# Performance work log

Hardware: AMD Instinct MI355X
Metric: run time of the kernel (lower is better)

The kernel has to match this reference:

```python
import jax, jax.numpy as jnp
import numpy as np

D_MODEL = 1024
NUM_HEADS = 16
D_K = D_MODEL // NUM_HEADS  # 64
THETA = 10000.0
BATCH = 2
SEQ = 2048


def _rope_tables(positions, d_k, theta):
    # freq_k = theta**(-2k/d_k), each repeated twice (interleaved layout)
    k = jnp.arange(d_k // 2, dtype=jnp.float32)
    freq = theta ** (-2.0 * k / d_k)            # [d_k/2]
    freq = jnp.repeat(freq, 2)                  # [d_k], pattern f0,f0,f1,f1,...
    ang = positions.astype(jnp.float32)[:, None] * freq[None, :]  # [s, d_k]
    return jnp.cos(ang), jnp.sin(ang)


def _apply_rope(x, cos, sin):
    # x: [b, h, s, d_k]; interleaved rotation: y[0::2]=-x[1::2], y[1::2]=x[0::2]
    x1 = x[..., 0::2]
    x2 = x[..., 1::2]
    y = jnp.stack([-x2, x1], axis=-1).reshape(x.shape)
    return x * cos + y * sin


def setup_inputs() -> dict:
    key = jax.random.key(0)
    kx, kq, kk, kv, ko = jax.random.split(key, 5)
    sw = (2.0 / (2 * D_MODEL)) ** 0.5
    return {
        "x": jax.random.normal(kx, (BATCH, SEQ, D_MODEL), dtype=jnp.float32),
        "WQ": jax.random.normal(kq, (D_MODEL, D_MODEL), dtype=jnp.float32) * sw,
        "WK": jax.random.normal(kk, (D_MODEL, D_MODEL), dtype=jnp.float32) * sw,
        "WV": jax.random.normal(kv, (D_MODEL, D_MODEL), dtype=jnp.float32) * sw,
        "WO": jax.random.normal(ko, (D_MODEL, D_MODEL), dtype=jnp.float32) * sw,
        "token_positions": jnp.arange(SEQ, dtype=jnp.int32),
    }


def reference(x, WQ, WK, WV, WO, token_positions):
    b, s, d_model = x.shape
    h, d_k = NUM_HEADS, D_K

    # fused QKV projection: W = cat([WQ,WK,WV], 0); QKV = x @ W.T
    W = jnp.concatenate([WQ, WK, WV], axis=0)          # [3*d_model, d_model]
    QKV = jnp.einsum('bsd,ed->bse', x, W)              # [b, s, 3*d_model]
    Q, K, V = jnp.split(QKV, 3, axis=-1)               # each [b, s, d_model]

    def to_heads(t):
        return t.reshape(b, s, h, d_k).transpose(0, 2, 1, 3)  # [b, h, s, d_k]

    Q, K, V = to_heads(Q), to_heads(K), to_heads(V)

    cos, sin = _rope_tables(token_positions, d_k, THETA)       # [s, d_k]
    Q = _apply_rope(Q, cos, sin)
    K = _apply_rope(K, cos, sin)

    scale = 1.0 / jnp.sqrt(jnp.float32(d_k))
    scores = jnp.einsum('bhqd,bhkd->bhqk', Q, K) * scale       # [b,h,s,s]
    causal = jnp.tril(jnp.ones((s, s), dtype=bool))
    scores = jnp.where(causal[None, None], scores, -jnp.inf)
    probs = jax.nn.softmax(scores, axis=-1)
    attn = jnp.einsum('bhqk,bhkd->bhqd', probs, V)             # [b,h,s,d_k]
    attn = attn.transpose(0, 2, 1, 3).reshape(b, s, h * d_k)   # [b,s,d_model]
    return jnp.einsum('bsd,ed->bse', attn, WO)                 # [b,s,d_model]
```

## Files before the change

kernel.cpp:

```cpp
#include <hip/hip_runtime.h>
#include <hip/hip_bf16.h>
#include <math.h>

#define BATCH 2
#define SEQ 2048
#define DMODEL 1024
#define NHEADS 16
#define DK 64
#define BH (BATCH*NHEADS)
#define GK 1024

#define SCALE2 0.18033688011112042f
#define SHIFT  16.0f

typedef __bf16 bf16_t;
typedef __bf16 bf16x8 __attribute__((ext_vector_type(8)));
typedef __bf16 bf16x4 __attribute__((ext_vector_type(4)));
typedef float  floatx4 __attribute__((ext_vector_type(4)));

__device__ __forceinline__ void load_lds16(const bf16_t* g, bf16_t* l) {
    __builtin_amdgcn_global_load_lds(
        (const __attribute__((address_space(1))) void*)g,
        (__attribute__((address_space(3))) void*)l,
        16, 0, 0);
}

__global__ __launch_bounds__(256) void rope_tables_kernel(
    const int* __restrict__ pos, float2* __restrict__ csT)
{
    int idx = blockIdx.x * 256 + threadIdx.x;
    int kk = idx & 31, s = idx >> 5;
    float freq = exp2f((float)kk * (-13.287712379549449f / 32.0f));
    float ang = (float)pos[s] * freq;
    float sn, cs;
    sincosf(ang, &sn, &cs);
    csT[idx] = make_float2(cs, sn);
}

__global__ __launch_bounds__(256) void convert_all_kernel(
    const float* __restrict__ x,
    const float* __restrict__ WQ, const float* __restrict__ WK,
    const float* __restrict__ WV, const float* __restrict__ WO,
    bf16_t* __restrict__ xb, bf16_t* __restrict__ Wb)
{
    const int blk = blockIdx.x;
    const float* src;
    bf16_t* dst;
    int base;
    if (blk < 2048) {
        src = x; dst = xb; base = blk * 2048;
    } else {
        int wi  = (blk - 2048) >> 9;
        base = ((blk - 2048) & 511) * 2048;
        src = (wi == 0) ? WQ : (wi == 1) ? WK : (wi == 2) ? WV : WO;
        dst = Wb + (size_t)wi * DMODEL * DMODEL;
    }
    int i = base + threadIdx.x * 8;
    float4 a = *(const float4*)(src + i);
    float4 b = *(const float4*)(src + i + 4);
    bf16x8 o;
    o[0] = (bf16_t)a.x; o[1] = (bf16_t)a.y; o[2] = (bf16_t)a.z; o[3] = (bf16_t)a.w;
    o[4] = (bf16_t)b.x; o[5] = (bf16_t)b.y; o[6] = (bf16_t)b.z; o[7] = (bf16_t)b.w;
    *(bf16x8*)(dst + i) = o;
}

__device__ __forceinline__ void gemm128_mainloop(
    const bf16_t* __restrict__ Arows, const bf16_t* __restrict__ Brows,
    bf16_t (*As)[32], bf16_t (*Bs)[32], int tid, floatx4 acc[4][4])
{
    const int lane = tid & 63;
    const int w = tid >> 6;
    const int wm = w >> 1, wn = w & 1;
    const int r = lane & 15, q = lane >> 4;

    const int row0 = tid >> 2,         kc0 = (tid & 3) << 3;
    const int row1 = (tid + 256) >> 2, kc1 = kc0;

    for (int kt = 0; kt < GK; kt += 32) {
        __syncthreads();
        load_lds16(Arows + (size_t)row0 * GK + kt + kc0, &As[row0][kc0]);
        load_lds16(Arows + (size_t)row1 * GK + kt + kc1, &As[row1][kc1]);
        load_lds16(Brows + (size_t)row0 * GK + kt + kc0, &Bs[row0][kc0]);
        load_lds16(Brows + (size_t)row1 * GK + kt + kc1, &Bs[row1][kc1]);
        __syncthreads();

        bf16x8 af[4], bfr[4];
        #pragma unroll
        for (int i = 0; i < 4; ++i)
            af[i] = *(const bf16x8*)&As[wm * 64 + i * 16 + r][q << 3];
        #pragma unroll
        for (int j = 0; j < 4; ++j)
            bfr[j] = *(const bf16x8*)&Bs[wn * 64 + j * 16 + r][q << 3];

        #pragma unroll
        for (int i = 0; i < 4; ++i)
            #pragma unroll
            for (int j = 0; j < 4; ++j)
                acc[i][j] = __builtin_amdgcn_mfma_f32_16x16x32_bf16(
                    af[i], bfr[j], acc[i][j], 0, 0, 0);
    }
}

__global__ __launch_bounds__(256) void qkv_gemm_kernel(
    const bf16_t* __restrict__ x, const bf16_t* __restrict__ Wb,
    const float2* __restrict__ csT,
    bf16_t* __restrict__ Qh, bf16_t* __restrict__ Kh, bf16_t* __restrict__ Vt)
{
    __shared__ __align__(16) char qsmem[128 * 136 * 2];
    bf16_t (*As)[32]  = (bf16_t(*)[32])qsmem;
    bf16_t (*Bs)[32]  = (bf16_t(*)[32])(qsmem + 8192);
    bf16_t (*Tt)[136] = (bf16_t(*)[136])qsmem;

    const int tid = threadIdx.x;
    const int m0 = blockIdx.y * 128;
    const int n0g = blockIdx.x * 128;
    const int which = n0g >> 10;
    const int nl0 = n0g & 1023;
    const bf16_t* Wsel = Wb + (size_t)which * DMODEL * DMODEL;

    floatx4 acc[4][4];
    #pragma unroll
    for (int i = 0; i < 4; ++i)
        #pragma unroll
        for (int j = 0; j < 4; ++j)
            acc[i][j] = (floatx4){0.f, 0.f, 0.f, 0.f};

    gemm128_mainloop(x + (size_t)m0 * GK, Wsel + (size_t)nl0 * GK, As, Bs, tid, acc);
    __syncthreads();

    const int w = tid >> 6, lane = tid & 63;
    const int wm = w >> 1, wn = w & 1;
    const int r = lane & 15, qd = lane >> 4;

    if (which < 2) {
        #pragma unroll
        for (int i = 0; i < 4; ++i)
            #pragma unroll
            for (int j = 0; j < 4; ++j)
                #pragma unroll
                for (int reg = 0; reg < 4; ++reg)
                    Tt[wm * 64 + i * 16 + qd * 4 + reg][wn * 64 + j * 16 + r] =
                        (bf16_t)acc[i][j][reg];
        __syncthreads();

        bf16_t* dst = (which == 0) ? Qh : Kh;
        #pragma unroll
        for (int k2 = 0; k2 < 8; ++k2) {
            int id = tid + 256 * k2;
            int rowm = id >> 4;
            int ch = id & 15;
            int m = m0 + rowm, b = m >> 11, s = m & 2047;
            int n = nl0 + ch * 8, h = n >> 6, dk = n & 63;
            bf16x8 v = *(const bf16x8*)&Tt[rowm][ch * 8];
            const float4* csp = (const float4*)&csT[(s << 5) + (dk >> 1)];
            float4 c01 = csp[0], c23 = csp[1];
            bf16x8 o;
            float e, od;
            e = (float)v[0]; od = (float)v[1];
            o[0] = (bf16_t)(e * c01.x - od * c01.y); o[1] = (bf16_t)(od * c01.x + e * c01.y);
            e = (float)v[2]; od = (float)v[3];
            o[2] = (bf16_t)(e * c01.z - od * c01.w); o[3] = (bf16_t)(od * c01.z + e * c01.w);
            e = (float)v[4]; od = (float)v[5];
            o[4] = (bf16_t)(e * c23.x - od * c23.y); o[5] = (bf16_t)(od * c23.x + e * c23.y);
            e = (float)v[6]; od = (float)v[7];
            o[6] = (bf16_t)(e * c23.z - od * c23.w); o[7] = (bf16_t)(od * c23.z + e * c23.w);
            *(bf16x8*)(dst + (((size_t)(b << 4) + h) * SEQ + s) * DK + dk) = o;
        }
    } else {
        #pragma unroll
        for (int i = 0; i < 4; ++i)
            #pragma unroll
            for (int j = 0; j < 4; ++j) {
                int n_local = wn * 64 + j * 16 + r;
                int m_base  = wm * 64 + i * 16 + qd * 4;
                bf16x4 t;
                #pragma unroll
                for (int reg = 0; reg < 4; ++reg) t[reg] = (bf16_t)acc[i][j][reg];
                *(bf16x4*)&Tt[n_local][m_base] = t;
            }
        __syncthreads();
        const int b = m0 >> 11, s0 = m0 & 2047;
        #pragma unroll
        for (int k2 = 0; k2 < 8; ++k2) {
            int id = tid + 256 * k2;
            int row = id >> 4;
            int ch  = id & 15;
            int n = nl0 + row, h = n >> 6, dk = n & 63;
            bf16x8 val = *(const bf16x8*)&Tt[row][ch * 8];
            *(bf16x8*)(Vt + (((size_t)(b << 4) + h) * DK + dk) * SEQ + s0 + ch * 8) = val;
        }
    }
}

__global__ __launch_bounds__(512, 4) void attn_mfma_kernel(
    const bf16_t* __restrict__ Qh, const bf16_t* __restrict__ Kh,
    const bf16_t* __restrict__ Vtg, bf16_t* __restrict__ attnO)
{
    __shared__ __align__(16) char smem[55296];
    bf16_t (*Ks)[64][72] = (bf16_t(*)[64][72])smem;
    bf16_t (*Vs)[64][72] = (bf16_t(*)[64][72])(smem + 18432);
    bf16_t (*ps)[16][72] = (bf16_t(*)[16][72])(smem + 36864);
    float  (*Om)[64][68] = (float(*)[64][68])smem;
    float  (*lsum)[64]   = (float(*)[64])(smem + 36864);

    const int tid = threadIdx.x, w = tid >> 6, lane = tid & 63;
    const int grp = w >> 2, wv = w & 3;
    const int r = lane & 15, qd = lane >> 4;
    const int bh = blockIdx.y;
    const int t = tid & 255;
    const int row0 = t >> 3, c80 = (t & 7) * 8;

    const bf16_t* Kbh = Kh  + (size_t)bh * SEQ * DK;
    const bf16_t* Vbh = Vtg + (size_t)bh * DK * SEQ;
    const int b = bh >> 4, h = bh & 15;

    for (int half = 0; half < 2; ++half) {
        const int qt = half ? (int)blockIdx.x : (31 - (int)blockIdx.x);
        const int q0 = qt * 64;
        const int nIter = (qt >> 1) + 1;

        const bf16_t* Qbase = Qh + (((size_t)bh * SEQ) + q0 + wv * 16 + r) * DK;
        bf16x8 aq0 = *(const bf16x8*)(Qbase + qd * 8);
        bf16x8 aq1 = *(const bf16x8*)(Qbase + 32 + qd * 8);

        int j0 = grp * 64;
        bf16x8 pk0 = *(const bf16x8*)(Kbh + (size_t)(j0 + row0) * DK + c80);
        bf16x8 pk1 = *(const bf16x8*)(Kbh + (size_t)(j0 + row0 + 32) * DK + c80);
        bf16x8 pv0 = *(const bf16x8*)(Vbh + (size_t)row0 * SEQ + j0 + c80);
        bf16x8 pv1 = *(const bf16x8*)(Vbh + (size_t)(row0 + 32) * SEQ + j0 + c80);

        floatx4 Oa[4];
        #pragma unroll
        for (int nd = 0; nd < 4; ++nd) Oa[nd] = (floatx4){0.f, 0.f, 0.f, 0.f};
        float l_lane[4] = {0.f, 0.f, 0.f, 0.f};

        for (int it = 0; it < nIter; ++it) {
            const int kb = 2 * it + grp;
            const bool active = (kb <= qt);
            __syncthreads();
            if (active) {
                *(bf16x8*)&Ks[grp][row0][c80]      = pk0;
                *(bf16x8*)&Ks[grp][row0 + 32][c80] = pk1;
                *(bf16x8*)&Vs[grp][row0][c80]      = pv0;
                *(bf16x8*)&Vs[grp][row0 + 32][c80] = pv1;
            }
            if (kb + 2 <= qt) {
                const int j0n = (kb + 2) * 64;
                pk0 = *(const bf16x8*)(Kbh + (size_t)(j0n + row0) * DK + c80);
                pk1 = *(const bf16x8*)(Kbh + (size_t)(j0n + row0 + 32) * DK + c80);
                pv0 = *(const bf16x8*)(Vbh + (size_t)row0 * SEQ + j0n + c80);
                pv1 = *(const bf16x8*)(Vbh + (size_t)(row0 + 32) * SEQ + j0n + c80);
            }
            __syncthreads();
            if (!active) continue;

            floatx4 acc[4];
            #pragma unroll
            for (int nt = 0; nt < 4; ++nt) {
                bf16x8 bk0 = *(const bf16x8*)&Ks[grp][nt * 16 + r][qd * 8];
                bf16x8 bk1 = *(const bf16x8*)&Ks[grp][nt * 16 + r][32 + qd * 8];
                floatx4 a = (floatx4){0.f, 0.f, 0.f, 0.f};
                a = __builtin_amdgcn_mfma_f32_16x16x32_bf16(aq0, bk0, a, 0, 0, 0);
                a = __builtin_amdgcn_mfma_f32_16x16x32_bf16(aq1, bk1, a, 0, 0, 0);
                acc[nt] = a;
            }

            const bool lastb = (kb == qt);
            #pragma unroll
            for (int nt = 0; nt < 4; ++nt)
                #pragma unroll
                for (int rg = 0; rg < 4; ++rg) {
                    float s2 = fmaf(acc[nt][rg], SCALE2, -SHIFT);
                    if (lastb && (nt * 16 + r > wv * 16 + qd * 4 + rg)) s2 = -200.0f;
                    float p = exp2f(s2);
                    acc[nt][rg] = p;
                    l_lane[rg] += p;
                }

            #pragma unroll
            for (int nt = 0; nt < 4; ++nt)
                #pragma unroll
                for (int rg = 0; rg < 4; ++rg)
                    ps[w][qd * 4 + rg][nt * 16 + r] = (bf16_t)acc[nt][rg];
            bf16x8 ap0 = *(const bf16x8*)&ps[w][r][qd * 8];
            bf16x8 ap1 = *(const bf16x8*)&ps[w][r][32 + qd * 8];

            #pragma unroll
            for (int nd = 0; nd < 4; ++nd) {
                bf16x8 bv0 = *(const bf16x8*)&Vs[grp][nd * 16 + r][qd * 8];
                bf16x8 bv1 = *(const bf16x8*)&Vs[grp][nd * 16 + r][32 + qd * 8];
                floatx4 c = Oa[nd];
                c = __builtin_amdgcn_mfma_f32_16x16x32_bf16(ap0, bv0, c, 0, 0, 0);
                c = __builtin_amdgcn_mfma_f32_16x16x32_bf16(ap1, bv1, c, 0, 0, 0);
                Oa[nd] = c;
            }
        }

        __syncthreads();
        #pragma unroll
        for (int rg = 0; rg < 4; ++rg) {
            float l = l_lane[rg];
            #pragma unroll
            for (int off = 1; off < 16; off <<= 1) l += __shfl_xor(l, off);
            int rowq = wv * 16 + qd * 4 + rg;
            if (r == 0) lsum[grp][rowq] = l;
            #pragma unroll
            for (int nd = 0; nd < 4; ++nd)
                Om[grp][rowq][nd * 16 + r] = Oa[nd][rg];
        }
        __syncthreads();
        {
            int rowq = tid >> 3, c8 = (tid & 7) * 8;
            float inv = 1.0f / (lsum[0][rowq] + lsum[1][rowq]);
            float4 a0 = *(const float4*)&Om[0][rowq][c8];
            float4 a1 = *(const float4*)&Om[0][rowq][c8 + 4];
            float4 b0 = *(const float4*)&Om[1][rowq][c8];
            float4 b1 = *(const float4*)&Om[1][rowq][c8 + 4];
            bf16x8 o;
            o[0] = (bf16_t)((a0.x + b0.x) * inv);
            o[1] = (bf16_t)((a0.y + b0.y) * inv);
            o[2] = (bf16_t)((a0.z + b0.z) * inv);
            o[3] = (bf16_t)((a0.w + b0.w) * inv);
            o[4] = (bf16_t)((a1.x + b1.x) * inv);
            o[5] = (bf16_t)((a1.y + b1.y) * inv);
            o[6] = (bf16_t)((a1.z + b1.z) * inv);
            o[7] = (bf16_t)((a1.w + b1.w) * inv);
            int s = q0 + rowq;
            *(bf16x8*)(attnO + ((size_t)b * SEQ + s) * DMODEL + (h << 6) + c8) = o;
        }
    }
}

__global__ __launch_bounds__(256) void out_gemm_kernel(
    const bf16_t* __restrict__ attnI, const bf16_t* __restrict__ WOb,
    float* __restrict__ out)
{
    __shared__ __align__(16) bf16_t As[64][32];
    __shared__ __align__(16) bf16_t Bs[128][32];

    const int tid = threadIdx.x;
    const int m0 = blockIdx.y * 64;
    const int n0 = blockIdx.x * 128;
    const int lane = tid & 63, w = tid >> 6;
    const int wm = w >> 1, wn = w & 1;
    const int r = lane & 15, q = lane >> 4;

    const bf16_t* Arows = attnI + (size_t)m0 * GK;
    const bf16_t* Brows = WOb + (size_t)n0 * GK;
    const int rowA = tid >> 2, kc = (tid & 3) << 3;
    const int rowB1 = (tid + 256) >> 2;

    floatx4 acc[2][4];
    #pragma unroll
    for (int i = 0; i < 2; ++i)
        #pragma unroll
        for (int j = 0; j < 4; ++j)
            acc[i][j] = (floatx4){0.f, 0.f, 0.f, 0.f};

    for (int kt = 0; kt < GK; kt += 32) {
        __syncthreads();
        load_lds16(Arows + (size_t)rowA * GK + kt + kc, &As[rowA][kc]);
        load_lds16(Brows + (size_t)rowA * GK + kt + kc, &Bs[rowA][kc]);
        load_lds16(Brows + (size_t)rowB1 * GK + kt + kc, &Bs[rowB1][kc]);
        __syncthreads();

        bf16x8 af[2], bfr[4];
        #pragma unroll
        for (int i = 0; i < 2; ++i)
            af[i] = *(const bf16x8*)&As[wm * 32 + i * 16 + r][q << 3];
        #pragma unroll
        for (int j = 0; j < 4; ++j)
            bfr[j] = *(const bf16x8*)&Bs[wn * 64 + j * 16 + r][q << 3];

        #pragma unroll
        for (int i = 0; i < 2; ++i)
            #pragma unroll
            for (int j = 0; j < 4; ++j)
                acc[i][j] = __builtin_amdgcn_mfma_f32_16x16x32_bf16(
                    af[i], bfr[j], acc[i][j], 0, 0, 0);
    }

    #pragma unroll
    for (int i = 0; i < 2; ++i)
        #pragma unroll
        for (int j = 0; j < 4; ++j)
            #pragma unroll
            for (int reg = 0; reg < 4; ++reg) {
                int m = m0 + wm * 32 + i * 16 + q * 4 + reg;
                int n = n0 + wn * 64 + j * 16 + r;
                out[(size_t)m * DMODEL + n] = acc[i][j][reg];
            }
}

extern "C" void kernel_launch(void* const* d_in, const int* in_sizes, int n_in,
                              void* d_out, int out_size, void* d_ws, size_t ws_size,
                              hipStream_t stream)
{
    (void)in_sizes; (void)n_in; (void)out_size; (void)ws_size;

    const float* x  = (const float*)d_in[0];
    const float* WQ = (const float*)d_in[1];
    const float* WK = (const float*)d_in[2];
    const float* WV = (const float*)d_in[3];
    const float* WO = (const float*)d_in[4];
    const int* tpos = (const int*)d_in[5];
    float* out = (float*)d_out;

    bf16_t* xb   = (bf16_t*)d_ws;
    bf16_t* Wb   = xb + (size_t)BATCH * SEQ * DMODEL;
    bf16_t* Qh   = Wb + (size_t)4 * DMODEL * DMODEL;
    bf16_t* Kh   = Qh + (size_t)BH * SEQ * DK;
    bf16_t* Vt   = Kh + (size_t)BH * SEQ * DK;
    bf16_t* attn = Vt + (size_t)BH * SEQ * DK;
    float2* csT  = (float2*)(attn + (size_t)BATCH * SEQ * DMODEL);

    rope_tables_kernel<<<dim3(SEQ * 32 / 256), dim3(256), 0, stream>>>(tpos, csT);

    convert_all_kernel<<<dim3(4096), dim3(256), 0, stream>>>(
        x, WQ, WK, WV, WO, xb, Wb);

    qkv_gemm_kernel<<<dim3(3 * DMODEL / 128, BATCH * SEQ / 128), dim3(256), 0, stream>>>(
        xb, Wb, csT, Qh, Kh, Vt);

    attn_mfma_kernel<<<dim3(16, 32), dim3(512), 0, stream>>>(Qh, Kh, Vt, attn);

    out_gemm_kernel<<<dim3(DMODEL / 128, BATCH * SEQ / 64), dim3(256), 0, stream>>>(
        attn, Wb + (size_t)3 * DMODEL * DMODEL, out);
}
```

Before: 184.3 us.

## Fuse rope-table build into conversion, co-process paired query tiles, split-K output GEMM

The rope cos/sin table is now built by extra blocks of the conversion kernel, which removes one launch. The attention kernel processes its high and low causal query tiles together in a single K/V loop, so each K/V tile loaded into LDS is reused by both tiles, at the cost of more registers and LDS. The output projection becomes a split-K GEMM with 128x128 tiles that writes two fp32 partials into a reused workspace, followed by a reduction kernel. This doubles the output traffic and adds a launch in exchange for larger tiles.

```diff
diff --git a/kernel.cpp b/kernel.cpp
--- a/kernel.cpp
+++ b/kernel.cpp
@@ -9,6 +9,8 @@
 #define DK 64
 #define BH (BATCH*NHEADS)
 #define GK 1024
+#define NX (BATCH*SEQ*DMODEL)
+#define NW (DMODEL*DMODEL)
 
 #define SCALE2 0.18033688011112042f
 #define SHIFT  16.0f
@@ -25,25 +27,24 @@
         16, 0, 0);
 }
 
-__global__ __launch_bounds__(256) void rope_tables_kernel(
-    const int* __restrict__ pos, float2* __restrict__ csT)
-{
-    int idx = blockIdx.x * 256 + threadIdx.x;
-    int kk = idx & 31, s = idx >> 5;
-    float freq = exp2f((float)kk * (-13.287712379549449f / 32.0f));
-    float ang = (float)pos[s] * freq;
-    float sn, cs;
-    sincosf(ang, &sn, &cs);
-    csT[idx] = make_float2(cs, sn);
-}
-
 __global__ __launch_bounds__(256) void convert_all_kernel(
     const float* __restrict__ x,
     const float* __restrict__ WQ, const float* __restrict__ WK,
     const float* __restrict__ WV, const float* __restrict__ WO,
-    bf16_t* __restrict__ xb, bf16_t* __restrict__ Wb)
+    const int* __restrict__ pos,
+    bf16_t* __restrict__ xb, bf16_t* __restrict__ Wb, float2* __restrict__ csT)
 {
     const int blk = blockIdx.x;
+    if (blk >= 4096) {
+        int idx = (blk - 4096) * 256 + threadIdx.x;
+        int kk = idx & 31, s = idx >> 5;
+        float freq = exp2f((float)kk * (-13.287712379549449f / 32.0f));
+        float ang = (float)pos[s] * freq;
+        float sn, cs;
+        sincosf(ang, &sn, &cs);
+        csT[idx] = make_float2(cs, sn);
+        return;
+    }
     const float* src;
     bf16_t* dst;
     int base;
@@ -53,7 +54,7 @@
         int wi  = (blk - 2048) >> 9;
         base = ((blk - 2048) & 511) * 2048;
         src = (wi == 0) ? WQ : (wi == 1) ? WK : (wi == 2) ? WV : WO;
-        dst = Wb + (size_t)wi * DMODEL * DMODEL;
+        dst = Wb + (size_t)wi * NW;
     }
     int i = base + threadIdx.x * 8;
     float4 a = *(const float4*)(src + i);
@@ -66,7 +67,7 @@
 
 __device__ __forceinline__ void gemm128_mainloop(
     const bf16_t* __restrict__ Arows, const bf16_t* __restrict__ Brows,
-    bf16_t (*As)[32], bf16_t (*Bs)[32], int tid, floatx4 acc[4][4])
+    bf16_t (*As)[32], bf16_t (*Bs)[32], int tid, floatx4 acc[4][4], int klen)
 {
     const int lane = tid & 63;
     const int w = tid >> 6;
@@ -76,7 +77,7 @@
     const int row0 = tid >> 2,         kc0 = (tid & 3) << 3;
     const int row1 = (tid + 256) >> 2, kc1 = kc0;
 
-    for (int kt = 0; kt < GK; kt += 32) {
+    for (int kt = 0; kt < klen; kt += 32) {
         __syncthreads();
         load_lds16(Arows + (size_t)row0 * GK + kt + kc0, &As[row0][kc0]);
         load_lds16(Arows + (size_t)row1 * GK + kt + kc1, &As[row1][kc1]);
@@ -116,7 +117,7 @@
     const int n0g = blockIdx.x * 128;
     const int which = n0g >> 10;
     const int nl0 = n0g & 1023;
-    const bf16_t* Wsel = Wb + (size_t)which * DMODEL * DMODEL;
+    const bf16_t* Wsel = Wb + (size_t)which * NW;
 
     floatx4 acc[4][4];
     #pragma unroll
@@ -125,7 +126,7 @@
         for (int j = 0; j < 4; ++j)
             acc[i][j] = (floatx4){0.f, 0.f, 0.f, 0.f};
 
-    gemm128_mainloop(x + (size_t)m0 * GK, Wsel + (size_t)nl0 * GK, As, Bs, tid, acc);
+    gemm128_mainloop(x + (size_t)m0 * GK, Wsel + (size_t)nl0 * GK, As, Bs, tid, acc, GK);
     __syncthreads();
 
     const int w = tid >> 6, lane = tid & 63;
@@ -147,8 +148,7 @@
         #pragma unroll
         for (int k2 = 0; k2 < 8; ++k2) {
             int id = tid + 256 * k2;
-            int rowm = id >> 4;
-            int ch = id & 15;
+            int rowm = id >> 4, ch = id & 15;
             int m = m0 + rowm, b = m >> 11, s = m & 2047;
             int n = nl0 + ch * 8, h = n >> 6, dk = n & 63;
             bf16x8 v = *(const bf16x8*)&Tt[rowm][ch * 8];
@@ -183,8 +183,7 @@
         #pragma unroll
         for (int k2 = 0; k2 < 8; ++k2) {
             int id = tid + 256 * k2;
-            int row = id >> 4;
-            int ch  = id & 15;
+            int row = id >> 4, ch = id & 15;
             int n = nl0 + row, h = n >> 6, dk = n & 63;
             bf16x8 val = *(const bf16x8*)&Tt[row][ch * 8];
             *(bf16x8*)(Vt + (((size_t)(b << 4) + h) * DK + dk) * SEQ + s0 + ch * 8) = val;
@@ -196,17 +195,19 @@
     const bf16_t* __restrict__ Qh, const bf16_t* __restrict__ Kh,
     const bf16_t* __restrict__ Vtg, bf16_t* __restrict__ attnO)
 {
-    __shared__ __align__(16) char smem[55296];
-    bf16_t (*Ks)[64][72] = (bf16_t(*)[64][72])smem;
-    bf16_t (*Vs)[64][72] = (bf16_t(*)[64][72])(smem + 18432);
-    bf16_t (*ps)[16][72] = (bf16_t(*)[16][72])(smem + 36864);
-    float  (*Om)[64][68] = (float(*)[64][68])smem;
-    float  (*lsum)[64]   = (float(*)[64])(smem + 36864);
+    __shared__ __align__(16) char smem[73728];
+    bf16_t (*Ks)[64][72]    = (bf16_t(*)[64][72])smem;
+    bf16_t (*Vs)[64][72]    = (bf16_t(*)[64][72])(smem + 18432);
+    bf16_t (*ps)[2][16][72] = (bf16_t(*)[2][16][72])(smem + 36864);
+    float  (*Om)[64][68]    = (float(*)[64][68])smem;
+    float  (*lsum)[64]      = (float(*)[64])(smem + 36864);
 
     const int tid = threadIdx.x, w = tid >> 6, lane = tid & 63;
     const int grp = w >> 2, wv = w & 3;
     const int r = lane & 15, qd = lane >> 4;
-    const int bh = blockIdx.y;
+    const int bh = blockIdx.y, bx = blockIdx.x;
+    const int qt_hi = 31 - bx, qt_lo = bx;
+    const int q0h = qt_hi * 64, q0l = qt_lo * 64;
     const int t = tid & 255;
     const int row0 = t >> 3, c80 = (t & 7) * 8;
 
@@ -214,99 +215,128 @@
     const bf16_t* Vbh = Vtg + (size_t)bh * DK * SEQ;
     const int b = bh >> 4, h = bh & 15;
 
-    for (int half = 0; half < 2; ++half) {
-        const int qt = half ? (int)blockIdx.x : (31 - (int)blockIdx.x);
-        const int q0 = qt * 64;
-        const int nIter = (qt >> 1) + 1;
-
-        const bf16_t* Qbase = Qh + (((size_t)bh * SEQ) + q0 + wv * 16 + r) * DK;
-        bf16x8 aq0 = *(const bf16x8*)(Qbase + qd * 8);
-        bf16x8 aq1 = *(const bf16x8*)(Qbase + 32 + qd * 8);
-
-        int j0 = grp * 64;
-        bf16x8 pk0 = *(const bf16x8*)(Kbh + (size_t)(j0 + row0) * DK + c80);
-        bf16x8 pk1 = *(const bf16x8*)(Kbh + (size_t)(j0 + row0 + 32) * DK + c80);
-        bf16x8 pv0 = *(const bf16x8*)(Vbh + (size_t)row0 * SEQ + j0 + c80);
-        bf16x8 pv1 = *(const bf16x8*)(Vbh + (size_t)(row0 + 32) * SEQ + j0 + c80);
-
-        floatx4 Oa[4];
-        #pragma unroll
-        for (int nd = 0; nd < 4; ++nd) Oa[nd] = (floatx4){0.f, 0.f, 0.f, 0.f};
-        float l_lane[4] = {0.f, 0.f, 0.f, 0.f};
-
-        for (int it = 0; it < nIter; ++it) {
-            const int kb = 2 * it + grp;
-            const bool active = (kb <= qt);
-            __syncthreads();
-            if (active) {
-                *(bf16x8*)&Ks[grp][row0][c80]      = pk0;
-                *(bf16x8*)&Ks[grp][row0 + 32][c80] = pk1;
-                *(bf16x8*)&Vs[grp][row0][c80]      = pv0;
-                *(bf16x8*)&Vs[grp][row0 + 32][c80] = pv1;
+    const bf16_t* Qbh = Qh + ((size_t)bh * SEQ + wv * 16 + r) * DK;
+    bf16x8 aqh0 = *(const bf16x8*)(Qbh + (size_t)q0h * DK + qd * 8);
+    bf16x8 aqh1 = *(const bf16x8*)(Qbh + (size_t)q0h * DK + 32 + qd * 8);
+    bf16x8 aql0 = *(const bf16x8*)(Qbh + (size_t)q0l * DK + qd * 8);
+    bf16x8 aql1 = *(const bf16x8*)(Qbh + (size_t)q0l * DK + 32 + qd * 8);
+
+    int j0 = grp * 64;
+    bf16x8 pk0 = *(const bf16x8*)(Kbh + (size_t)(j0 + row0) * DK + c80);
+    bf16x8 pk1 = *(const bf16x8*)(Kbh + (size_t)(j0 + row0 + 32) * DK + c80);
+    bf16x8 pv0 = *(const bf16x8*)(Vbh + (size_t)row0 * SEQ + j0 + c80);
+    bf16x8 pv1 = *(const bf16x8*)(Vbh + (size_t)(row0 + 32) * SEQ + j0 + c80);
+
+    floatx4 Oh[4], Ol[4];
+    #pragma unroll
+    for (int nd = 0; nd < 4; ++nd) {
+        Oh[nd] = (floatx4){0.f, 0.f, 0.f, 0.f};
+        Ol[nd] = (floatx4){0.f, 0.f, 0.f, 0.f};
+    }
+    float lh[4] = {0.f, 0.f, 0.f, 0.f}, ll[4] = {0.f, 0.f, 0.f, 0.f};
+
+    const int nIter = (qt_hi >> 1) + 1;
+    for (int it = 0; it < nIter; ++it) {
+        const int kb = 2 * it + grp;
+        const bool act = (kb <= qt_hi);
+        const bool lo_act = (kb <= qt_lo);
+        __syncthreads();
+        if (act) {
+            *(bf16x8*)&Ks[grp][row0][c80]      = pk0;
+            *(bf16x8*)&Ks[grp][row0 + 32][c80] = pk1;
+            *(bf16x8*)&Vs[grp][row0][c80]      = pv0;
+            *(bf16x8*)&Vs[grp][row0 + 32][c80] = pv1;
+        }
+        if (kb + 2 <= qt_hi) {
+            const int j0n = (kb + 2) * 64;
+            pk0 = *(const bf16x8*)(Kbh + (size_t)(j0n + row0) * DK + c80);
+            pk1 = *(const bf16x8*)(Kbh + (size_t)(j0n + row0 + 32) * DK + c80);
+            pv0 = *(const bf16x8*)(Vbh + (size_t)row0 * SEQ + j0n + c80);
+            pv1 = *(const bf16x8*)(Vbh + (size_t)(row0 + 32) * SEQ + j0n + c80);
+        }
+        __syncthreads();
+        if (!act) continue;
+
+        floatx4 ah[4], al[4];
+        #pragma unroll
+        for (int nt = 0; nt < 4; ++nt) {
+            bf16x8 bk0 = *(const bf16x8*)&Ks[grp][nt * 16 + r][qd * 8];
+            bf16x8 bk1 = *(const bf16x8*)&Ks[grp][nt * 16 + r][32 + qd * 8];
+            floatx4 a = (floatx4){0.f, 0.f, 0.f, 0.f};
+            a = __builtin_amdgcn_mfma_f32_16x16x32_bf16(aqh0, bk0, a, 0, 0, 0);
+            a = __builtin_amdgcn_mfma_f32_16x16x32_bf16(aqh1, bk1, a, 0, 0, 0);
+            ah[nt] = a;
+            if (lo_act) {
+                floatx4 a2 = (floatx4){0.f, 0.f, 0.f, 0.f};
+                a2 = __builtin_amdgcn_mfma_f32_16x16x32_bf16(aql0, bk0, a2, 0, 0, 0);
+                a2 = __builtin_amdgcn_mfma_f32_16x16x32_bf16(aql1, bk1, a2, 0, 0, 0);
+                al[nt] = a2;
             }
-            if (kb + 2 <= qt) {
-                const int j0n = (kb + 2) * 64;
-                pk0 = *(const bf16x8*)(Kbh + (size_t)(j0n + row0) * DK + c80);
-                pk1 = *(const bf16x8*)(Kbh + (size_t)(j0n + row0 + 32) * DK + c80);
-                pv0 = *(const bf16x8*)(Vbh + (size_t)row0 * SEQ + j0n + c80);
-                pv1 = *(const bf16x8*)(Vbh + (size_t)(row0 + 32) * SEQ + j0n + c80);
+        }
+
+        const bool dh = (kb == qt_hi);
+        #pragma unroll
+        for (int nt = 0; nt < 4; ++nt)
+            #pragma unroll
+            for (int rg = 0; rg < 4; ++rg) {
+                float s2 = fmaf(ah[nt][rg], SCALE2, -SHIFT);
+                if (dh && (nt * 16 + r > wv * 16 + qd * 4 + rg)) s2 = -200.0f;
+                float p = exp2f(s2);
+                lh[rg] += p;
+                ps[w][0][qd * 4 + rg][nt * 16 + r] = (bf16_t)p;
             }
-            __syncthreads();
-            if (!active) continue;
-
-            floatx4 acc[4];
-            #pragma unroll
-            for (int nt = 0; nt < 4; ++nt) {
-                bf16x8 bk0 = *(const bf16x8*)&Ks[grp][nt * 16 + r][qd * 8];
-                bf16x8 bk1 = *(const bf16x8*)&Ks[grp][nt * 16 + r][32 + qd * 8];
-                floatx4 a = (floatx4){0.f, 0.f, 0.f, 0.f};
-                a = __builtin_amdgcn_mfma_f32_16x16x32_bf16(aq0, bk0, a, 0, 0, 0);
-                a = __builtin_amdgcn_mfma_f32_16x16x32_bf16(aq1, bk1, a, 0, 0, 0);
-                acc[nt] = a;
-            }
-
-            const bool lastb = (kb == qt);
+        if (lo_act) {
+            const bool dl = (kb == qt_lo);
             #pragma unroll
             for (int nt = 0; nt < 4; ++nt)
                 #pragma unroll
                 for (int rg = 0; rg < 4; ++rg) {
-                    float s2 = fmaf(acc[nt][rg], SCALE2, -SHIFT);
-                    if (lastb && (nt * 16 + r > wv * 16 + qd * 4 + rg)) s2 = -200.0f;
+                    float s2 = fmaf(al[nt][rg], SCALE2, -SHIFT);
+                    if (dl && (nt * 16 + r > wv * 16 + qd * 4 + rg)) s2 = -200.0f;
                     float p = exp2f(s2);
-                    acc[nt][rg] = p;
-                    l_lane[rg] += p;
+                    ll[rg] += p;
+                    ps[w][1][qd * 4 + rg][nt * 16 + r] = (bf16_t)p;
                 }
-
-            #pragma unroll
-            for (int nt = 0; nt < 4; ++nt)
-                #pragma unroll
-                for (int rg = 0; rg < 4; ++rg)
-                    ps[w][qd * 4 + rg][nt * 16 + r] = (bf16_t)acc[nt][rg];
-            bf16x8 ap0 = *(const bf16x8*)&ps[w][r][qd * 8];
-            bf16x8 ap1 = *(const bf16x8*)&ps[w][r][32 + qd * 8];
-
-            #pragma unroll
-            for (int nd = 0; nd < 4; ++nd) {
-                bf16x8 bv0 = *(const bf16x8*)&Vs[grp][nd * 16 + r][qd * 8];
-                bf16x8 bv1 = *(const bf16x8*)&Vs[grp][nd * 16 + r][32 + qd * 8];
-                floatx4 c = Oa[nd];
-                c = __builtin_amdgcn_mfma_f32_16x16x32_bf16(ap0, bv0, c, 0, 0, 0);
-                c = __builtin_amdgcn_mfma_f32_16x16x32_bf16(ap1, bv1, c, 0, 0, 0);
-                Oa[nd] = c;
+        }
+        bf16x8 aph0 = *(const bf16x8*)&ps[w][0][r][qd * 8];
+        bf16x8 aph1 = *(const bf16x8*)&ps[w][0][r][32 + qd * 8];
+        bf16x8 apl0, apl1;
+        if (lo_act) {
+            apl0 = *(const bf16x8*)&ps[w][1][r][qd * 8];
+            apl1 = *(const bf16x8*)&ps[w][1][r][32 + qd * 8];
+        }
+
+        #pragma unroll
+        for (int nd = 0; nd < 4; ++nd) {
+            bf16x8 bv0 = *(const bf16x8*)&Vs[grp][nd * 16 + r][qd * 8];
+            bf16x8 bv1 = *(const bf16x8*)&Vs[grp][nd * 16 + r][32 + qd * 8];
+            floatx4 c = Oh[nd];
+            c = __builtin_amdgcn_mfma_f32_16x16x32_bf16(aph0, bv0, c, 0, 0, 0);
+            c = __builtin_amdgcn_mfma_f32_16x16x32_bf16(aph1, bv1, c, 0, 0, 0);
+            Oh[nd] = c;
+            if (lo_act) {
+                floatx4 c2 = Ol[nd];
+                c2 = __builtin_amdgcn_mfma_f32_16x16x32_bf16(apl0, bv0, c2, 0, 0, 0);
+                c2 = __builtin_amdgcn_mfma_f32_16x16x32_bf16(apl1, bv1, c2, 0, 0, 0);
+                Ol[nd] = c2;
             }
         }
-
-        __syncthreads();
+    }
+
+    #pragma unroll
+    for (int tsel = 0; tsel < 2; ++tsel) {
+        __syncthreads();
+        const int q0 = tsel ? q0l : q0h;
         #pragma unroll
         for (int rg = 0; rg < 4; ++rg) {
-            float l = l_lane[rg];
+            float l = tsel ? ll[rg] : lh[rg];
             #pragma unroll
             for (int off = 1; off < 16; off <<= 1) l += __shfl_xor(l, off);
             int rowq = wv * 16 + qd * 4 + rg;
             if (r == 0) lsum[grp][rowq] = l;
             #pragma unroll
             for (int nd = 0; nd < 4; ++nd)
-                Om[grp][rowq][nd * 16 + r] = Oa[nd][rg];
+                Om[grp][rowq][nd * 16 + r] = tsel ? Ol[nd][rg] : Oh[nd][rg];
         }
         __syncthreads();
         {
@@ -331,65 +361,53 @@
     }
 }
 
-__global__ __launch_bounds__(256) void out_gemm_kernel(
+__global__ __launch_bounds__(256) void out_gemm_partial(
     const bf16_t* __restrict__ attnI, const bf16_t* __restrict__ WOb,
-    float* __restrict__ out)
-{
-    __shared__ __align__(16) bf16_t As[64][32];
+    float* __restrict__ P)
+{
+    __shared__ __align__(16) bf16_t As[128][32];
     __shared__ __align__(16) bf16_t Bs[128][32];
 
     const int tid = threadIdx.x;
-    const int m0 = blockIdx.y * 64;
+    const int m0 = blockIdx.y * 128;
     const int n0 = blockIdx.x * 128;
-    const int lane = tid & 63, w = tid >> 6;
+    const int kh = blockIdx.z;
+
+    floatx4 acc[4][4];
+    #pragma unroll
+    for (int i = 0; i < 4; ++i)
+        #pragma unroll
+        for (int j = 0; j < 4; ++j)
+            acc[i][j] = (floatx4){0.f, 0.f, 0.f, 0.f};
+
+    gemm128_mainloop(attnI + (size_t)m0 * GK + kh * 512,
+                     WOb + (size_t)n0 * GK + kh * 512, As, Bs, tid, acc, 512);
+
+    float* Pd = P + (size_t)kh * NX;
+    const int w = tid >> 6, lane = tid & 63;
     const int wm = w >> 1, wn = w & 1;
     const int r = lane & 15, q = lane >> 4;
 
-    const bf16_t* Arows = attnI + (size_t)m0 * GK;
-    const bf16_t* Brows = WOb + (size_t)n0 * GK;
-    const int rowA = tid >> 2, kc = (tid & 3) << 3;
-    const int rowB1 = (tid + 256) >> 2;
-
-    floatx4 acc[2][4];
     #pragma unroll
-    for (int i = 0; i < 2; ++i)
+    for (int i = 0; i < 4; ++i)
         #pragma unroll
         for (int j = 0; j < 4; ++j)
-            acc[i][j] = (floatx4){0.f, 0.f, 0.f, 0.f};
-
-    for (int kt = 0; kt < GK; kt += 32) {
-        __syncthreads();
-        load_lds16(Arows + (size_t)rowA * GK + kt + kc, &As[rowA][kc]);
-        load_lds16(Brows + (size_t)rowA * GK + kt + kc, &Bs[rowA][kc]);
-        load_lds16(Brows + (size_t)rowB1 * GK + kt + kc, &Bs[rowB1][kc]);
-        __syncthreads();
-
-        bf16x8 af[2], bfr[4];
-        #pragma unroll
-        for (int i = 0; i < 2; ++i)
-            af[i] = *(const bf16x8*)&As[wm * 32 + i * 16 + r][q << 3];
-        #pragma unroll
-        for (int j = 0; j < 4; ++j)
-            bfr[j] = *(const bf16x8*)&Bs[wn * 64 + j * 16 + r][q << 3];
-
-        #pragma unroll
-        for (int i = 0; i < 2; ++i)
-            #pragma unroll
-            for (int j = 0; j < 4; ++j)
-                acc[i][j] = __builtin_amdgcn_mfma_f32_16x16x32_bf16(
-                    af[i], bfr[j], acc[i][j], 0, 0, 0);
-    }
-
-    #pragma unroll
-    for (int i = 0; i < 2; ++i)
-        #pragma unroll
-        for (int j = 0; j < 4; ++j)
             #pragma unroll
             for (int reg = 0; reg < 4; ++reg) {
-                int m = m0 + wm * 32 + i * 16 + q * 4 + reg;
+                int m = m0 + wm * 64 + i * 16 + q * 4 + reg;
                 int n = n0 + wn * 64 + j * 16 + r;
-                out[(size_t)m * DMODEL + n] = acc[i][j][reg];
+                Pd[(size_t)m * DMODEL + n] = acc[i][j][reg];
             }
+}
+
+__global__ __launch_bounds__(256) void reduce_out_kernel(
+    const float* __restrict__ P, float* __restrict__ out)
+{
+    size_t i = ((size_t)blockIdx.x * 256 + threadIdx.x) * 4;
+    float4 a = *(const float4*)(P + i);
+    float4 b = *(const float4*)(P + (size_t)NX + i);
+    float4 c = make_float4(a.x + b.x, a.y + b.y, a.z + b.z, a.w + b.w);
+    *(float4*)(out + i) = c;
 }
 
 extern "C" void kernel_launch(void* const* d_in, const int* in_sizes, int n_in,
@@ -406,24 +424,25 @@
     const int* tpos = (const int*)d_in[5];
     float* out = (float*)d_out;
 
-    bf16_t* xb   = (bf16_t*)d_ws;
-    bf16_t* Wb   = xb + (size_t)BATCH * SEQ * DMODEL;
-    bf16_t* Qh   = Wb + (size_t)4 * DMODEL * DMODEL;
+    bf16_t* Wb   = (bf16_t*)d_ws;
+    float2* csT  = (float2*)(Wb + (size_t)4 * NW);
+    bf16_t* attn = (bf16_t*)(csT + SEQ * 32);
+    bf16_t* xb   = attn + (size_t)NX;
+    bf16_t* Qh   = xb + (size_t)NX;
     bf16_t* Kh   = Qh + (size_t)BH * SEQ * DK;
     bf16_t* Vt   = Kh + (size_t)BH * SEQ * DK;
-    bf16_t* attn = Vt + (size_t)BH * SEQ * DK;
-    float2* csT  = (float2*)(attn + (size_t)BATCH * SEQ * DMODEL);
-
-    rope_tables_kernel<<<dim3(SEQ * 32 / 256), dim3(256), 0, stream>>>(tpos, csT);
-
-    convert_all_kernel<<<dim3(4096), dim3(256), 0, stream>>>(
-        x, WQ, WK, WV, WO, xb, Wb);
+    float*  P    = (float*)xb;
+
+    convert_all_kernel<<<dim3(4352), dim3(256), 0, stream>>>(
+        x, WQ, WK, WV, WO, tpos, xb, Wb, csT);
 
     qkv_gemm_kernel<<<dim3(3 * DMODEL / 128, BATCH * SEQ / 128), dim3(256), 0, stream>>>(
         xb, Wb, csT, Qh, Kh, Vt);
 
     attn_mfma_kernel<<<dim3(16, 32), dim3(512), 0, stream>>>(Qh, Kh, Vt, attn);
 
-    out_gemm_kernel<<<dim3(DMODEL / 128, BATCH * SEQ / 64), dim3(256), 0, stream>>>(
-        attn, Wb + (size_t)3 * DMODEL * DMODEL, out);
-}
+    out_gemm_partial<<<dim3(DMODEL / 128, BATCH * SEQ / 128, 2), dim3(256), 0, stream>>>(
+        attn, Wb + (size_t)3 * NW, P);
+
+    reduce_out_kernel<<<dim3(4096), dim3(256), 0, stream>>>(P, out);
+}
```

Result: slower. 216.2 us (+17.3%).
